# Performance work log

Hardware: AMD Instinct MI355X
Metric: run time of the kernel (lower is better)

## Reference

```python
import jax, jax.numpy as jnp
import numpy as np

B, K, D = 8, 2048, 1024

def setup_inputs() -> dict:
    key = jax.random.key(0)
    k1, k2 = jax.random.split(key)
    x = jax.random.normal(k1, (B, K, D), dtype=jnp.float32)
    W = jax.random.normal(k2, (K, K), dtype=jnp.float32) * 0.02  # dt_proj weight [out=K, in=K]
    b = jnp.zeros((K,), dtype=jnp.float32)                        # dt_proj bias
    return {"x": x, "W": W, "b": b}

def _scan_combine(c1, c2):
    # compose affine maps s -> a*s + u; (a1,u1) then (a2,u2)
    a1, u1 = c1
    a2, u2 = c2
    return (a2 * a1, a2 * u1 + u2)

def reference(x, W, b):
    # lam[b,t,d] = sigmoid( sum_k x[b,k,d] * W[t,k] + b[t] )
    # (dt_proj is a Linear over the TIME axis after permute(0,2,1))
    lam = jax.nn.sigmoid(jnp.einsum('bkd,tk->btd', x, W) + b[None, :, None])
    # s_t = lam_t * s_{t-1} + (1 - lam_t) * x_t, s_0 = 0  -> associative scan over time
    _, ys = jax.lax.associative_scan(_scan_combine, (lam, (1.0 - lam) * x), axis=1)
    return ys
```

## Files before the change

### kernel.cpp

```cpp
#include <hip/hip_runtime.h>
#include <hip/hip_bf16.h>
#include <stdint.h>

#define B_ 8
#define K_ 2048
#define D_ 1024
#define NC 32
#define TC (K_ / NC)

typedef float v4f __attribute__((ext_vector_type(4)));
typedef short v8s __attribute__((ext_vector_type(8)));

__device__ __forceinline__ unsigned short f2bf(float f) {
    __hip_bfloat16 h = __float2bfloat16(f);
    return *reinterpret_cast<unsigned short*>(&h);
}

__device__ __forceinline__ void async_ld16(const void* g, void* l) {
    __builtin_amdgcn_global_load_lds(
        (__attribute__((address_space(1))) void*)(void*)g,
        (__attribute__((address_space(3))) void*)l,
        16, 0, 0);
}

__global__ void conv_w(const float* __restrict__ W, unsigned short* __restrict__ Wb) {
    int i = (blockIdx.x * 256 + threadIdx.x) * 4;
    float4 v = *(const float4*)(W + i);
    ushort4 o;
    o.x = f2bf(v.x); o.y = f2bf(v.y); o.z = f2bf(v.z); o.w = f2bf(v.w);
    *(ushort4*)(Wb + i) = o;
}

__global__ void conv_x_t(const float* __restrict__ x, unsigned short* __restrict__ xT) {
    const int k0 = blockIdx.x * 64, d0 = blockIdx.y * 64, bb = blockIdx.z;
    __shared__ unsigned short tile[64][68];
    const int tid = threadIdx.x;
    const int tx = tid & 15, ty = tid >> 4;
    const float* xp = x + (size_t)bb * K_ * D_;
#pragma unroll
    for (int r = 0; r < 4; r++) {
        int row = ty + r * 16;
        float4 v = *(const float4*)(xp + (size_t)(k0 + row) * D_ + d0 + tx * 4);
        tile[row][tx * 4 + 0] = f2bf(v.x);
        tile[row][tx * 4 + 1] = f2bf(v.y);
        tile[row][tx * 4 + 2] = f2bf(v.z);
        tile[row][tx * 4 + 3] = f2bf(v.w);
    }
    __syncthreads();
    unsigned short* op = xT + (size_t)bb * D_ * K_;
#pragma unroll
    for (int r = 0; r < 4; r++) {
        int dcol = ty + r * 16;
        ushort4 u;
        u.x = tile[tx * 4 + 0][dcol];
        u.y = tile[tx * 4 + 1][dcol];
        u.z = tile[tx * 4 + 2][dcol];
        u.w = tile[tx * 4 + 3][dcol];
        *(ushort4*)(op + (size_t)(d0 + dcol) * K_ + k0 + tx * 4) = u;
    }
}

__launch_bounds__(256)
__global__ void gemm_sig(const unsigned short* __restrict__ Wb,
                         const unsigned short* __restrict__ xT,
                         const float* __restrict__ bias,
                         float* __restrict__ lam) {
    const int tM = blockIdx.x, tN = blockIdx.y, bb = blockIdx.z;
    __shared__ unsigned short As[2][128 * 32];
    __shared__ unsigned short Bs[2][128 * 32];
    const int tid = threadIdx.x;
    const int w = tid >> 6;
    const int lane = tid & 63;
    const int wm = w >> 1, wn = w & 1;
    const int quad = lane >> 4;
    const int l16 = lane & 15;

    v4f acc[4][4];
#pragma unroll
    for (int i = 0; i < 4; i++)
#pragma unroll
        for (int j = 0; j < 4; j++) acc[i][j] = (v4f)0.f;

    const unsigned short* Ag = Wb + (size_t)(tM * 128) * K_;
    const unsigned short* Bg = xT + (size_t)bb * D_ * K_ + (size_t)(tN * 128) * K_;

    const int srow = lane >> 2;
    const int schunk = (lane & 3) * 8;

    for (int k0 = 0; k0 < K_; k0 += 64) {
#pragma unroll
        for (int h = 0; h < 2; h++) {
#pragma unroll
            for (int q = 0; q < 2; q++) {
                int rb = (q * 4 + w) * 16;
                async_ld16(Ag + (size_t)(rb + srow) * K_ + k0 + h * 32 + schunk, &As[h][rb * 32]);
                async_ld16(Bg + (size_t)(rb + srow) * K_ + k0 + h * 32 + schunk, &Bs[h][rb * 32]);
            }
        }
        __syncthreads();
#pragma unroll
        for (int h = 0; h < 2; h++) {
            v8s af[4], bfr[4];
#pragma unroll
            for (int i = 0; i < 4; i++)
                af[i] = *(const v8s*)(&As[h][(wm * 64 + i * 16 + l16) * 32 + quad * 8]);
#pragma unroll
            for (int j = 0; j < 4; j++)
                bfr[j] = *(const v8s*)(&Bs[h][(wn * 64 + j * 16 + l16) * 32 + quad * 8]);
#pragma unroll
            for (int i = 0; i < 4; i++)
#pragma unroll
                for (int j = 0; j < 4; j++)
                    acc[i][j] = __builtin_amdgcn_mfma_f32_16x16x32_bf16(af[i], bfr[j], acc[i][j], 0, 0, 0);
        }
        __syncthreads();
    }

    float* out = lam + (size_t)bb * K_ * D_;
#pragma unroll
    for (int i = 0; i < 4; i++) {
        int rowb = tM * 128 + wm * 64 + i * 16 + quad * 4;
#pragma unroll
        for (int r = 0; r < 4; r++) {
            float bt = bias[rowb + r];
#pragma unroll
            for (int j = 0; j < 4; j++) {
                int col = tN * 128 + wn * 64 + j * 16 + l16;
                float v = acc[i][j][r] + bt;
                out[(size_t)(rowb + r) * D_ + col] = 1.f / (1.f + __expf(-v));
            }
        }
    }
}

__global__ void scan_pass1(const float* __restrict__ lam, const float* __restrict__ x,
                           float* __restrict__ Ac, float* __restrict__ Uc) {
    int id = blockIdx.x * 256 + threadIdx.x;
    int d2 = (id & 511) * 2;
    int c = (id >> 9) & (NC - 1);
    int bb = id >> 14;
    const float* lp = lam + ((size_t)bb * K_ + (size_t)c * TC) * D_ + d2;
    const float* xp = x   + ((size_t)bb * K_ + (size_t)c * TC) * D_ + d2;
    float2 A = make_float2(1.f, 1.f), U = make_float2(0.f, 0.f);
#pragma unroll 8
    for (int t = 0; t < TC; t++) {
        float2 l  = *(const float2*)(lp + (size_t)t * D_);
        float2 xv = *(const float2*)(xp + (size_t)t * D_);
        A.x *= l.x; A.y *= l.y;
        U.x = l.x * U.x + (1.f - l.x) * xv.x;
        U.y = l.y * U.y + (1.f - l.y) * xv.y;
    }
    size_t oi = ((size_t)bb * NC + c) * D_ + d2;
    *(float2*)(Ac + oi) = A;
    *(float2*)(Uc + oi) = U;
}

__global__ void scan_pass2(const float* __restrict__ Ac, const float* __restrict__ Uc,
                           float* __restrict__ Sin) {
    int id = blockIdx.x * 256 + threadIdx.x;
    int d = id & (D_ - 1);
    int bb = id >> 10;
    float s = 0.f;
#pragma unroll
    for (int c = 0; c < NC; c++) {
        int idx = (bb * NC + c) * D_ + d;
        Sin[idx] = s;
        s = Ac[idx] * s + Uc[idx];
    }
}

__global__ void scan_pass3(const float* __restrict__ x, const float* __restrict__ Sin,
                           float* __restrict__ lamout) {
    int id = blockIdx.x * 256 + threadIdx.x;
    int d2 = (id & 511) * 2;
    int c = (id >> 9) & (NC - 1);
    int bb = id >> 14;
    float* lp = lamout + ((size_t)bb * K_ + (size_t)c * TC) * D_ + d2;
    const float* xp = x + ((size_t)bb * K_ + (size_t)c * TC) * D_ + d2;
    size_t si = ((size_t)bb * NC + c) * D_ + d2;
    float2 s = *(const float2*)(Sin + si);
#pragma unroll 8
    for (int t = 0; t < TC; t++) {
        float2 l  = *(const float2*)(lp + (size_t)t * D_);
        float2 xv = *(const float2*)(xp + (size_t)t * D_);
        s.x = l.x * s.x + (1.f - l.x) * xv.x;
        s.y = l.y * s.y + (1.f - l.y) * xv.y;
        *(float2*)(lp + (size_t)t * D_) = s;
    }
}

extern "C" void kernel_launch(void* const* d_in, const int* in_sizes, int n_in,
                              void* d_out, int out_size, void* d_ws, size_t ws_size,
                              hipStream_t stream) {
    const float* x    = (const float*)d_in[0];
    const float* W    = (const float*)d_in[1];
    const float* bias = (const float*)d_in[2];
    float* out = (float*)d_out;
    char* ws = (char*)d_ws;

    unsigned short* xT = (unsigned short*)ws;
    unsigned short* Wb = (unsigned short*)(ws + 33554432);
    float* Ac  = (float*)(ws + 33554432);
    float* Uc  = (float*)(ws + 33554432 + 1048576);
    float* Sin = (float*)(ws + 33554432 + 2097152);

    conv_w<<<dim3(K_ * K_ / 4 / 256), 256, 0, stream>>>(W, Wb);
    conv_x_t<<<dim3(K_ / 64, D_ / 64, B_), 256, 0, stream>>>(x, xT);
    gemm_sig<<<dim3(K_ / 128, D_ / 128, B_), 256, 0, stream>>>(Wb, xT, bias, out);
    scan_pass1<<<dim3(B_ * NC * D_ / 2 / 256), 256, 0, stream>>>(out, x, Ac, Uc);
    scan_pass2<<<dim3(B_ * D_ / 256), 256, 0, stream>>>(Ac, Uc, Sin);
    scan_pass3<<<dim3(B_ * NC * D_ / 2 / 256), 256, 0, stream>>>(x, Sin, out);
}
```

Before: 277.3 us.

## Store lambda as transposed fp16, scan from bf16 xT, fuse scan passes

The GEMM epilogue now writes lambda as fp16 in a transposed [b,d,t] layout instead of fp32 [b,t,d]. The scan passes read lambda and the already-built bf16 xT contiguously along time with 16-byte vector loads, which cuts scan read traffic. The chunk-carry pass is merged into the final pass: each thread recomputes its prefix serially from the chunk summaries. The two conversion kernels are merged into one launch and the chunk count is doubled. The scan now reads x in bf16 and lambda in fp16 rather than fp32, which adds precision risk, and the strided transposed 8-byte stores in the epilogue may write inefficiently.

Measured after the change: 298.9 us. +7.8%, slower.

```diff
diff --git a/kernel.cpp b/kernel.cpp
--- a/kernel.cpp
+++ b/kernel.cpp
@@ -1,19 +1,32 @@
 #include <hip/hip_runtime.h>
 #include <hip/hip_bf16.h>
+#include <hip/hip_fp16.h>
 #include <stdint.h>
 
 #define B_ 8
 #define K_ 2048
 #define D_ 1024
-#define NC 32
+#define NC 64
 #define TC (K_ / NC)
 
 typedef float v4f __attribute__((ext_vector_type(4)));
 typedef short v8s __attribute__((ext_vector_type(8)));
+typedef unsigned short v8u __attribute__((ext_vector_type(8)));
 
 __device__ __forceinline__ unsigned short f2bf(float f) {
     __hip_bfloat16 h = __float2bfloat16(f);
     return *reinterpret_cast<unsigned short*>(&h);
+}
+__device__ __forceinline__ float bf2f(unsigned short u) {
+    uint32_t v = (uint32_t)u << 16;
+    float f;
+    __builtin_memcpy(&f, &v, 4);
+    return f;
+}
+__device__ __forceinline__ float h2f(unsigned short u) {
+    __half h;
+    __builtin_memcpy(&h, &u, 2);
+    return __half2float(h);
 }
 
 __device__ __forceinline__ void async_ld16(const void* g, void* l) {
@@ -23,18 +36,20 @@
         16, 0, 0);
 }
 
-__global__ void conv_w(const float* __restrict__ W, unsigned short* __restrict__ Wb) {
-    int i = (blockIdx.x * 256 + threadIdx.x) * 4;
-    float4 v = *(const float4*)(W + i);
-    ushort4 o;
-    o.x = f2bf(v.x); o.y = f2bf(v.y); o.z = f2bf(v.z); o.w = f2bf(v.w);
-    *(ushort4*)(Wb + i) = o;
-}
-
-__global__ void conv_x_t(const float* __restrict__ x, unsigned short* __restrict__ xT) {
-    const int k0 = blockIdx.x * 64, d0 = blockIdx.y * 64, bb = blockIdx.z;
+__global__ void conv_fused(const float* __restrict__ x, const float* __restrict__ W,
+                           unsigned short* __restrict__ xT, unsigned short* __restrict__ Wb) {
+    const int blk = blockIdx.x;
+    const int tid = threadIdx.x;
+    if (blk >= 4096) {
+        int i = ((blk - 4096) * 256 + tid) * 4;
+        float4 v = *(const float4*)(W + i);
+        ushort4 o;
+        o.x = f2bf(v.x); o.y = f2bf(v.y); o.z = f2bf(v.z); o.w = f2bf(v.w);
+        *(ushort4*)(Wb + i) = o;
+        return;
+    }
+    const int k0 = (blk & 31) * 64, d0 = ((blk >> 5) & 15) * 64, bb = blk >> 9;
     __shared__ unsigned short tile[64][68];
-    const int tid = threadIdx.x;
     const int tx = tid & 15, ty = tid >> 4;
     const float* xp = x + (size_t)bb * K_ * D_;
 #pragma unroll
@@ -64,7 +79,7 @@
 __global__ void gemm_sig(const unsigned short* __restrict__ Wb,
                          const unsigned short* __restrict__ xT,
                          const float* __restrict__ bias,
-                         float* __restrict__ lam) {
+                         unsigned short* __restrict__ lamT) {
     const int tM = blockIdx.x, tN = blockIdx.y, bb = blockIdx.z;
     __shared__ unsigned short As[2][128 * 32];
     __shared__ unsigned short Bs[2][128 * 32];
@@ -116,76 +131,82 @@
         __syncthreads();
     }
 
-    float* out = lam + (size_t)bb * K_ * D_;
+    unsigned short* lt = lamT + (size_t)bb * D_ * K_;
 #pragma unroll
     for (int i = 0; i < 4; i++) {
         int rowb = tM * 128 + wm * 64 + i * 16 + quad * 4;
-#pragma unroll
-        for (int r = 0; r < 4; r++) {
-            float bt = bias[rowb + r];
-#pragma unroll
-            for (int j = 0; j < 4; j++) {
-                int col = tN * 128 + wn * 64 + j * 16 + l16;
-                float v = acc[i][j][r] + bt;
-                out[(size_t)(rowb + r) * D_ + col] = 1.f / (1.f + __expf(-v));
-            }
-        }
-    }
-}
-
-__global__ void scan_pass1(const float* __restrict__ lam, const float* __restrict__ x,
+        float4 bv = *(const float4*)(bias + rowb);
+#pragma unroll
+        for (int j = 0; j < 4; j++) {
+            int col = tN * 128 + wn * 64 + j * 16 + l16;
+            float s0 = 1.f / (1.f + __expf(-(acc[i][j][0] + bv.x)));
+            float s1 = 1.f / (1.f + __expf(-(acc[i][j][1] + bv.y)));
+            float s2 = 1.f / (1.f + __expf(-(acc[i][j][2] + bv.z)));
+            float s3 = 1.f / (1.f + __expf(-(acc[i][j][3] + bv.w)));
+            union { __half2 h[2]; uint2 u; } pk;
+            pk.h[0] = __float22half2_rn(make_float2(s0, s1));
+            pk.h[1] = __float22half2_rn(make_float2(s2, s3));
+            *(uint2*)(lt + (size_t)col * K_ + rowb) = pk.u;
+        }
+    }
+}
+
+__global__ void scan_pass1(const unsigned short* __restrict__ lamT,
+                           const unsigned short* __restrict__ xT,
                            float* __restrict__ Ac, float* __restrict__ Uc) {
     int id = blockIdx.x * 256 + threadIdx.x;
-    int d2 = (id & 511) * 2;
-    int c = (id >> 9) & (NC - 1);
-    int bb = id >> 14;
-    const float* lp = lam + ((size_t)bb * K_ + (size_t)c * TC) * D_ + d2;
-    const float* xp = x   + ((size_t)bb * K_ + (size_t)c * TC) * D_ + d2;
-    float2 A = make_float2(1.f, 1.f), U = make_float2(0.f, 0.f);
-#pragma unroll 8
-    for (int t = 0; t < TC; t++) {
-        float2 l  = *(const float2*)(lp + (size_t)t * D_);
-        float2 xv = *(const float2*)(xp + (size_t)t * D_);
-        A.x *= l.x; A.y *= l.y;
-        U.x = l.x * U.x + (1.f - l.x) * xv.x;
-        U.y = l.y * U.y + (1.f - l.y) * xv.y;
-    }
-    size_t oi = ((size_t)bb * NC + c) * D_ + d2;
-    *(float2*)(Ac + oi) = A;
-    *(float2*)(Uc + oi) = U;
-}
-
-__global__ void scan_pass2(const float* __restrict__ Ac, const float* __restrict__ Uc,
-                           float* __restrict__ Sin) {
+    int d = id & (D_ - 1);
+    int c = (id >> 10) & (NC - 1);
+    int bb = id >> 16;
+    size_t base = ((size_t)bb * D_ + d) * K_ + (size_t)c * TC;
+    const unsigned short* lp = lamT + base;
+    const unsigned short* xp = xT + base;
+    float A = 1.f, U = 0.f;
+#pragma unroll
+    for (int u = 0; u < TC / 8; u++) {
+        v8u lv = *(const v8u*)(lp + u * 8);
+        v8u xv = *(const v8u*)(xp + u * 8);
+#pragma unroll
+        for (int e = 0; e < 8; e++) {
+            float l = h2f(lv[e]);
+            float xf = bf2f(xv[e]);
+            A *= l;
+            U = l * U + (1.f - l) * xf;
+        }
+    }
+    int oi = (bb * NC + c) * D_ + d;
+    Ac[oi] = A;
+    Uc[oi] = U;
+}
+
+__global__ void scan_pass23(const unsigned short* __restrict__ lamT,
+                            const unsigned short* __restrict__ xT,
+                            const float* __restrict__ Ac, const float* __restrict__ Uc,
+                            float* __restrict__ out) {
     int id = blockIdx.x * 256 + threadIdx.x;
     int d = id & (D_ - 1);
-    int bb = id >> 10;
+    int c = (id >> 10) & (NC - 1);
+    int bb = id >> 16;
     float s = 0.f;
-#pragma unroll
-    for (int c = 0; c < NC; c++) {
-        int idx = (bb * NC + c) * D_ + d;
-        Sin[idx] = s;
-        s = Ac[idx] * s + Uc[idx];
-    }
-}
-
-__global__ void scan_pass3(const float* __restrict__ x, const float* __restrict__ Sin,
-                           float* __restrict__ lamout) {
-    int id = blockIdx.x * 256 + threadIdx.x;
-    int d2 = (id & 511) * 2;
-    int c = (id >> 9) & (NC - 1);
-    int bb = id >> 14;
-    float* lp = lamout + ((size_t)bb * K_ + (size_t)c * TC) * D_ + d2;
-    const float* xp = x + ((size_t)bb * K_ + (size_t)c * TC) * D_ + d2;
-    size_t si = ((size_t)bb * NC + c) * D_ + d2;
-    float2 s = *(const float2*)(Sin + si);
-#pragma unroll 8
-    for (int t = 0; t < TC; t++) {
-        float2 l  = *(const float2*)(lp + (size_t)t * D_);
-        float2 xv = *(const float2*)(xp + (size_t)t * D_);
-        s.x = l.x * s.x + (1.f - l.x) * xv.x;
-        s.y = l.y * s.y + (1.f - l.y) * xv.y;
-        *(float2*)(lp + (size_t)t * D_) = s;
+    for (int cc = 0; cc < c; cc++) {
+        int ai = (bb * NC + cc) * D_ + d;
+        s = Ac[ai] * s + Uc[ai];
+    }
+    size_t base = ((size_t)bb * D_ + d) * K_ + (size_t)c * TC;
+    const unsigned short* lp = lamT + base;
+    const unsigned short* xp = xT + base;
+    float* op = out + ((size_t)bb * K_ + (size_t)c * TC) * D_ + d;
+#pragma unroll
+    for (int u = 0; u < TC / 8; u++) {
+        v8u lv = *(const v8u*)(lp + u * 8);
+        v8u xv = *(const v8u*)(xp + u * 8);
+#pragma unroll
+        for (int e = 0; e < 8; e++) {
+            float l = h2f(lv[e]);
+            float xf = bf2f(xv[e]);
+            s = l * s + (1.f - l) * xf;
+            op[(size_t)(u * 8 + e) * D_] = s;
+        }
     }
 }
 
@@ -198,16 +219,15 @@
     float* out = (float*)d_out;
     char* ws = (char*)d_ws;
 
-    unsigned short* xT = (unsigned short*)ws;
-    unsigned short* Wb = (unsigned short*)(ws + 33554432);
-    float* Ac  = (float*)(ws + 33554432);
-    float* Uc  = (float*)(ws + 33554432 + 1048576);
-    float* Sin = (float*)(ws + 33554432 + 2097152);
-
-    conv_w<<<dim3(K_ * K_ / 4 / 256), 256, 0, stream>>>(W, Wb);
-    conv_x_t<<<dim3(K_ / 64, D_ / 64, B_), 256, 0, stream>>>(x, xT);
-    gemm_sig<<<dim3(K_ / 128, D_ / 128, B_), 256, 0, stream>>>(Wb, xT, bias, out);
-    scan_pass1<<<dim3(B_ * NC * D_ / 2 / 256), 256, 0, stream>>>(out, x, Ac, Uc);
-    scan_pass2<<<dim3(B_ * D_ / 256), 256, 0, stream>>>(Ac, Uc, Sin);
-    scan_pass3<<<dim3(B_ * NC * D_ / 2 / 256), 256, 0, stream>>>(x, Sin, out);
-}
+    const size_t MB = 1024 * 1024;
+    unsigned short* xT   = (unsigned short*)ws;
+    unsigned short* Wb   = (unsigned short*)(ws + 32 * MB);
+    float* Ac = (float*)(ws + 32 * MB);
+    float* Uc = (float*)(ws + 34 * MB);
+    unsigned short* lamT = (unsigned short*)(ws + 40 * MB);
+
+    conv_fused<<<dim3(8192), 256, 0, stream>>>(x, W, xT, Wb);
+    gemm_sig<<<dim3(K_ / 128, D_ / 128, B_), 256, 0, stream>>>(Wb, xT, bias, lamT);
+    scan_pass1<<<dim3(B_ * NC * D_ / 256), 256, 0, stream>>>(lamT, xT, Ac, Uc);
+    scan_pass23<<<dim3(B_ * NC * D_ / 256), 256, 0, stream>>>(lamT, xT, Ac, Uc, out);
+}
```
